# Kernel optimization log

Measured on AMD Instinct MI355X. Metric: run time of the kernel, lower is better.

The kernel has to match this reference:

```python
import jax, jax.numpy as jnp
import numpy as np
import math

EMBED_DIM = 512
NHEAD = 8
HEAD_DIM = EMBED_DIM // NHEAD
B, L = 32, 512
EPS = 1e-5


def layer_norm(x, gamma, beta):
    mu = jnp.mean(x, axis=-1, keepdims=True)
    var = jnp.var(x, axis=-1, keepdims=True)
    return (x - mu) * jax.lax.rsqrt(var + EPS) * gamma + beta


def setup_inputs() -> dict:
    key = jax.random.key(0)
    ks = jax.random.split(key, 16)
    D = EMBED_DIM
    s = 1.0 / math.sqrt(D)
    return {
        "x": jax.random.normal(ks[0], (B, L, D), dtype=jnp.float32),
        "inter": jax.random.normal(ks[1], (B, L, L, 4), dtype=jnp.float32),
        "qkv_w": jax.random.normal(ks[2], (D, 3 * D), dtype=jnp.float32) * s,
        "qkv_b": jnp.zeros((3 * D,), dtype=jnp.float32),
        "out_w": jax.random.normal(ks[3], (D, D), dtype=jnp.float32) * s,
        "out_b": jnp.zeros((D,), dtype=jnp.float32),
        "norm1_g": jnp.ones((D,), dtype=jnp.float32),
        "norm1_b": jnp.zeros((D,), dtype=jnp.float32),
        "norm2_g": jnp.ones((D,), dtype=jnp.float32),
        "norm2_b": jnp.zeros((D,), dtype=jnp.float32),
        "inter_w": jax.random.normal(ks[4], (4, NHEAD), dtype=jnp.float32) * 0.5,
        "ffn_w1": jax.random.normal(ks[5], (D, 4 * D), dtype=jnp.float32) * s,
        "ffn_b1": jnp.zeros((4 * D,), dtype=jnp.float32),
        "ffn_w2": jax.random.normal(ks[6], (4 * D, D), dtype=jnp.float32) * (1.0 / math.sqrt(4 * D)),
        "ffn_b2": jnp.zeros((D,), dtype=jnp.float32),
    }


def reference(x, inter, qkv_w, qkv_b, out_w, out_b, norm1_g, norm1_b,
              norm2_g, norm2_b, inter_w, ffn_w1, ffn_b1, ffn_w2, ffn_b2):
    Bb, Ll, D = x.shape
    residual = x
    h = layer_norm(x, norm1_g, norm1_b)
    qkv = (h @ qkv_w + qkv_b).reshape(Bb, Ll, 3, NHEAD, HEAD_DIM)
    qkv = jnp.transpose(qkv, (2, 0, 3, 1, 4))  # (3, B, H, L, hd)
    q, k, v = qkv[0], qkv[1], qkv[2]
    scale = math.sqrt(HEAD_DIM)
    scores = jnp.einsum("bhqd,bhkd->bhqk", q, k) / scale
    # pairwise interaction bias: (B,L,L,4) @ (4,H) -> (B,H,L,L)
    bias = jnp.einsum("bqkf,fh->bhqk", inter, inter_w)
    attn = jax.nn.softmax(scores + bias, axis=-1)
    # dropout p=0 in eval mode
    out = jnp.einsum("bhqk,bhkd->bhqd", attn, v)
    out = jnp.transpose(out, (0, 2, 1, 3)).reshape(Bb, Ll, D)
    x = residual + out @ out_w + out_b
    h2 = layer_norm(x, norm2_g, norm2_b)
    ffn = jax.nn.gelu(h2 @ ffn_w1 + ffn_b1, approximate=False) @ ffn_w2 + ffn_b2
    return x + ffn
```

## Files before the change

kernel.cpp:

```cpp
#include <hip/hip_runtime.h>
#include <math.h>

#define BB 32
#define LL 512
#define DD 512
#define NH 8
#define HD 64

typedef __attribute__((ext_vector_type(8))) short bf16x8;
typedef __attribute__((ext_vector_type(4))) float f32x4;

__device__ __forceinline__ unsigned short f2bf(float x) {
    union { float f; unsigned u; } v; v.f = x;
    unsigned r = v.u + 0x7fffu + ((v.u >> 16) & 1u);
    return (unsigned short)(r >> 16);
}

__device__ __forceinline__ float warp_sum(float v) {
    #pragma unroll
    for (int o = 32; o > 0; o >>= 1) v += __shfl_down(v, o);
    return v;
}

__global__ void ln_kernel(const float* __restrict__ X, const float* __restrict__ g,
                          const float* __restrict__ b, unsigned short* __restrict__ Y) {
    __shared__ float red[8];
    const size_t base = (size_t)blockIdx.x * DD;
    const int t = threadIdx.x;
    float x0 = X[base + t], x1 = X[base + t + 256];
    float s = warp_sum(x0 + x1);
    float q = warp_sum(x0 * x0 + x1 * x1);
    if ((t & 63) == 0) { red[t >> 6] = s; red[4 + (t >> 6)] = q; }
    __syncthreads();
    float S = red[0] + red[1] + red[2] + red[3];
    float Q = red[4] + red[5] + red[6] + red[7];
    float mu  = S * (1.0f / 512.0f);
    float var = Q * (1.0f / 512.0f) - mu * mu;
    float r = rsqrtf(var + 1e-5f);
    Y[base + t]       = f2bf((x0 - mu) * r * g[t] + b[t]);
    Y[base + t + 256] = f2bf((x1 - mu) * r * g[t + 256] + b[t + 256]);
}

__global__ void transpose_bf16(const float* __restrict__ W, unsigned short* __restrict__ WT,
                               int K, int N) {
    __shared__ float t[32][33];
    const int n0 = blockIdx.x * 32, k0 = blockIdx.y * 32;
    const int tx = threadIdx.x & 31, ty = threadIdx.x >> 5;
    #pragma unroll
    for (int r = 0; r < 32; r += 8)
        t[ty + r][tx] = W[(size_t)(k0 + ty + r) * N + n0 + tx];
    __syncthreads();
    #pragma unroll
    for (int r = 0; r < 32; r += 8)
        WT[(size_t)(n0 + ty + r) * K + k0 + tx] = f2bf(t[tx][ty + r]);
}

template <int ACT, int RES, int OM>
__global__ __launch_bounds__(256)
void gemm_mfma(const unsigned short* __restrict__ A, const unsigned short* __restrict__ BT,
               const float* __restrict__ bias, const float* __restrict__ res,
               void* __restrict__ Cv, unsigned short* __restrict__ kfrag,
               unsigned short* __restrict__ vfrag, int M, int N, int K) {
    __shared__ unsigned short As0[128 * 64];
    __shared__ unsigned short Bs0[128 * 64];
    __shared__ unsigned short As1[128 * 64];
    __shared__ unsigned short Bs1[128 * 64];
    const int tid = threadIdx.x;
    const int wave = tid >> 6, lane = tid & 63;
    const int wm = (wave >> 1) * 64, wn = (wave & 1) * 64;

    const int nx = N >> 7;
    const int chunk = (int)gridDim.x >> 3;
    const int o = ((int)blockIdx.x & 7) * chunk + ((int)blockIdx.x >> 3);
    const int bn = (o % nx) * 128;
    const int bm = (o / nx) * 128;

    f32x4 acc[4][4] = {};

    auto stage = [&](unsigned short* AS, unsigned short* BS, int k0) {
        #pragma unroll
        for (int it = 0; it < 4; ++it) {
            const int s = it * 256 + tid;
            const int row = s >> 3, pch = s & 7;
            const int lch = pch ^ (row & 7);
            const unsigned short* ga = A + (size_t)(bm + row) * K + k0 + lch * 8;
            __builtin_amdgcn_global_load_lds(
                (const __attribute__((address_space(1))) void*)ga,
                (__attribute__((address_space(3))) void*)(AS + s * 8), 16, 0, 0);
            const unsigned short* gb = BT + (size_t)(bn + row) * K + k0 + lch * 8;
            __builtin_amdgcn_global_load_lds(
                (const __attribute__((address_space(1))) void*)gb,
                (__attribute__((address_space(3))) void*)(BS + s * 8), 16, 0, 0);
        }
    };

    auto compute = [&](const unsigned short* AS, const unsigned short* BS) {
        #pragma unroll
        for (int ks = 0; ks < 2; ++ks) {
            bf16x8 af[4], bfr[4];
            #pragma unroll
            for (int i = 0; i < 4; ++i) {
                const int row = wm + i * 16 + (lane & 15);
                const int pch = (ks * 4 + (lane >> 4)) ^ (row & 7);
                af[i] = *(const bf16x8*)(AS + row * 64 + pch * 8);
            }
            #pragma unroll
            for (int j = 0; j < 4; ++j) {
                const int row = wn + j * 16 + (lane & 15);
                const int pch = (ks * 4 + (lane >> 4)) ^ (row & 7);
                bfr[j] = *(const bf16x8*)(BS + row * 64 + pch * 8);
            }
            #pragma unroll
            for (int i = 0; i < 4; ++i)
                #pragma unroll
                for (int j = 0; j < 4; ++j)
                    acc[i][j] = __builtin_amdgcn_mfma_f32_16x16x32_bf16(
                        af[i], bfr[j], acc[i][j], 0, 0, 0);
        }
    };

    stage(As0, Bs0, 0);
    for (int k0 = 0; k0 < K; k0 += 128) {
        __syncthreads();
        if (k0 + 64 < K) stage(As1, Bs1, k0 + 64);
        compute(As0, Bs0);
        __syncthreads();
        if (k0 + 128 < K) stage(As0, Bs0, k0 + 128);
        compute(As1, Bs1);
    }

    const int cl = lane & 15, rq = (lane >> 4) * 4;
    #pragma unroll
    for (int j = 0; j < 4; ++j) {
        const int col = bn + wn + j * 16 + cl;
        const float bv = bias[col];
        #pragma unroll
        for (int i = 0; i < 4; ++i) {
            const int r0 = bm + wm + i * 16 + rq;
            #pragma unroll
            for (int r = 0; r < 4; ++r) {
                float v = acc[i][j][r] + bv;
                if (ACT == 1) v = 0.5f * v * (1.0f + erff(v * 0.70710678118654752f));
                if (RES) v += res[(size_t)(r0 + r) * N + col];
                if (OM == 0) {
                    ((float*)Cv)[(size_t)(r0 + r) * N + col] = v;
                } else if (OM == 1) {
                    ((unsigned short*)Cv)[(size_t)(r0 + r) * N + col] = f2bf(v);
                } else {
                    const int row = r0 + r;
                    const int b = row >> 9, kpos = row & 511;
                    if (col < 512) {
                        ((unsigned short*)Cv)[(size_t)row * 512 + col] = f2bf(v * 0.125f);
                    } else if (col < 1024) {
                        const int h = (col - 512) >> 6, dd = (col - 512) & 63;
                        const int kt = kpos >> 6, jj = (kpos >> 4) & 3, lo2 = kpos & 15;
                        const int kk = dd >> 5, hi2 = (dd >> 3) & 3, e = dd & 7;
                        kfrag[((((size_t)(b * NH + h) * 8 + kt) * 2 + kk) * 4 + jj) * 512
                              + (hi2 * 16 + lo2) * 8 + e] = f2bf(v);
                    } else {
                        const int h = (col - 1024) >> 6, dd = (col - 1024) & 63;
                        const int kt = kpos >> 6, kk = (kpos >> 5) & 1, hi2 = (kpos >> 3) & 3, e = kpos & 7;
                        const int jj = dd >> 4, lo2 = dd & 15;
                        vfrag[((((size_t)(b * NH + h) * 8 + kt) * 2 + kk) * 4 + jj) * 512
                              + (hi2 * 16 + lo2) * 8 + e] = f2bf(v);
                    }
                }
            }
        }
    }
}

__global__ __launch_bounds__(512)
void flash_kernel(const unsigned short* __restrict__ qbuf,
                  const unsigned short* __restrict__ kfrag,
                  const unsigned short* __restrict__ vfrag,
                  const float* __restrict__ inter,
                  const float* __restrict__ iw,
                  unsigned short* __restrict__ O) {
    __shared__ float it[2][16 * 256];
    __shared__ unsigned short plds[8][16 * 72];
    const int qg = blockIdx.x, b = blockIdx.y;
    const int tid = threadIdx.x, wave = tid >> 6, lane = tid & 63;
    const int h = wave;
    const int lo = lane & 15, hi = lane >> 4;

    const float iw0 = iw[h], iw1 = iw[8 + h], iw2 = iw[16 + h], iw3 = iw[24 + h];
    const float* interb = inter + (size_t)b * 512 * 512 * 4;
    unsigned short* pw = &plds[wave][0];

    const unsigned short* qp = qbuf + ((size_t)(b * 512 + qg * 16 + lo)) * 512 + h * 64 + hi * 8;
    const bf16x8 qf0 = *(const bf16x8*)(qp);
    const bf16x8 qf1 = *(const bf16x8*)(qp + 32);

    const unsigned short* kfb = kfrag + (size_t)(b * NH + h) * 32768 + (size_t)lane * 8;
    const unsigned short* vfb = vfrag + (size_t)(b * NH + h) * 32768 + (size_t)lane * 8;

    const int srow0 = wave * 2, srow1 = wave * 2 + 1;
    const float* sg0 = interb + (((size_t)(qg * 16 + srow0)) * 512 + (lane ^ (srow0 & 7))) * 4;
    const float* sg1 = interb + (((size_t)(qg * 16 + srow1)) * 512 + (lane ^ (srow1 & 7))) * 4;

    f32x4 o[4] = {};
    float m = -1e30f, lsum = 0.0f;

    bf16x8 kf[8];
    #pragma unroll
    for (int jj = 0; jj < 8; ++jj)
        kf[jj] = *(const bf16x8*)(kfb + jj * 512);
    __builtin_amdgcn_global_load_lds(
        (const __attribute__((address_space(1))) void*)sg0,
        (__attribute__((address_space(3))) void*)(&it[0][srow0 * 256] + lane * 4), 16, 0, 0);
    __builtin_amdgcn_global_load_lds(
        (const __attribute__((address_space(1))) void*)sg1,
        (__attribute__((address_space(3))) void*)(&it[0][srow1 * 256] + lane * 4), 16, 0, 0);

    #pragma unroll 1
    for (int kt = 0; kt < 8; ++kt) {
        const int buf = kt & 1;
        __syncthreads();
        f32x4 s4[4] = {};
        __builtin_amdgcn_s_setprio(1);
        #pragma unroll
        for (int j = 0; j < 4; ++j)
            s4[j] = __builtin_amdgcn_mfma_f32_16x16x32_bf16(kf[j], qf0, s4[j], 0, 0, 0);
        #pragma unroll
        for (int j = 0; j < 4; ++j)
            s4[j] = __builtin_amdgcn_mfma_f32_16x16x32_bf16(kf[4 + j], qf1, s4[j], 0, 0, 0);
        __builtin_amdgcn_s_setprio(0);
        const unsigned short* vp = vfb + kt * 4096;
        bf16x8 vf[8];
        #pragma unroll
        for (int jj = 0; jj < 8; ++jj)
            vf[jj] = *(const bf16x8*)(vp + jj * 512);
        if (kt < 7) {
            const unsigned short* kp = kfb + (kt + 1) * 4096;
            #pragma unroll
            for (int jj = 0; jj < 8; ++jj)
                kf[jj] = *(const bf16x8*)(kp + jj * 512);
        }
        if (kt < 7) {
            const int kb2 = (kt + 1) * 64;
            __builtin_amdgcn_global_load_lds(
                (const __attribute__((address_space(1))) void*)(sg0 + kb2 * 4),
                (__attribute__((address_space(3))) void*)(&it[buf ^ 1][srow0 * 256] + lane * 4),
                16, 0, 0);
            __builtin_amdgcn_global_load_lds(
                (const __attribute__((address_space(1))) void*)(sg1 + kb2 * 4),
                (__attribute__((address_space(3))) void*)(&it[buf ^ 1][srow1 * 256] + lane * 4),
                16, 0, 0);
        }
        __builtin_amdgcn_sched_barrier(0);
        {
            const float* bb = &it[buf][lo * 256];
            const int x7 = lo & 7;
            #pragma unroll
            for (int j = 0; j < 4; ++j) {
                #pragma unroll
                for (int r = 0; r < 4; ++r) {
                    const int c = (((hi * 4 + r) ^ x7) + j * 16) * 4;
                    const float4 f = *(const float4*)(bb + c);
                    s4[j][r] = s4[j][r] + f.x * iw0 + f.y * iw1 + f.z * iw2 + f.w * iw3;
                }
            }
        }
        float t0 = fmaxf(fmaxf(s4[0][0], s4[0][1]), fmaxf(s4[0][2], s4[0][3]));
        float t1 = fmaxf(fmaxf(s4[1][0], s4[1][1]), fmaxf(s4[1][2], s4[1][3]));
        float t2 = fmaxf(fmaxf(s4[2][0], s4[2][1]), fmaxf(s4[2][2], s4[2][3]));
        float t3 = fmaxf(fmaxf(s4[3][0], s4[3][1]), fmaxf(s4[3][2], s4[3][3]));
        float mx = fmaxf(fmaxf(t0, t1), fmaxf(t2, t3));
        mx = fmaxf(mx, __shfl_xor(mx, 16));
        mx = fmaxf(mx, __shfl_xor(mx, 32));
        const float mn = fmaxf(m, mx);
        const float al = __expf(m - mn);
        m = mn;
        #pragma unroll
        for (int j = 0; j < 4; ++j)
            #pragma unroll
            for (int r = 0; r < 4; ++r)
                s4[j][r] = __expf(s4[j][r] - mn);
        float u0 = (s4[0][0] + s4[0][1]) + (s4[0][2] + s4[0][3]);
        float u1 = (s4[1][0] + s4[1][1]) + (s4[1][2] + s4[1][3]);
        float u2 = (s4[2][0] + s4[2][1]) + (s4[2][2] + s4[2][3]);
        float u3 = (s4[3][0] + s4[3][1]) + (s4[3][2] + s4[3][3]);
        float ts = (u0 + u1) + (u2 + u3);
        ts += __shfl_xor(ts, 16);
        ts += __shfl_xor(ts, 32);
        lsum = lsum * al + ts;
        const float aR0 = __shfl(al, hi * 4 + 0);
        const float aR1 = __shfl(al, hi * 4 + 1);
        const float aR2 = __shfl(al, hi * 4 + 2);
        const float aR3 = __shfl(al, hi * 4 + 3);
        #pragma unroll
        for (int j2 = 0; j2 < 4; ++j2) {
            o[j2][0] *= aR0; o[j2][1] *= aR1; o[j2][2] *= aR2; o[j2][3] *= aR3;
        }
        uint2* pq = (uint2*)(pw + lo * 72);
        #pragma unroll
        for (int j = 0; j < 4; ++j) {
            uint2 d;
            d.x = (unsigned)f2bf(s4[j][0]) | ((unsigned)f2bf(s4[j][1]) << 16);
            d.y = (unsigned)f2bf(s4[j][2]) | ((unsigned)f2bf(s4[j][3]) << 16);
            pq[j * 4 + hi] = d;
        }
        __builtin_amdgcn_s_setprio(1);
        #pragma unroll
        for (int kk = 0; kk < 2; ++kk) {
            const bf16x8 pf = *(const bf16x8*)(pw + lo * 72 + kk * 32 + hi * 8);
            #pragma unroll
            for (int j2 = 0; j2 < 4; ++j2)
                o[j2] = __builtin_amdgcn_mfma_f32_16x16x32_bf16(
                    pf, vf[kk * 4 + j2], o[j2], 0, 0, 0);
        }
        __builtin_amdgcn_s_setprio(0);
    }

    const float iR0 = 1.0f / __shfl(lsum, hi * 4 + 0);
    const float iR1 = 1.0f / __shfl(lsum, hi * 4 + 1);
    const float iR2 = 1.0f / __shfl(lsum, hi * 4 + 2);
    const float iR3 = 1.0f / __shfl(lsum, hi * 4 + 3);
    const int qC0 = qg * 16 + hi * 4;
    #pragma unroll
    for (int j2 = 0; j2 < 4; ++j2) {
        O[(size_t)(b * 512 + qC0 + 0) * 512 + h * 64 + j2 * 16 + lo] = f2bf(o[j2][0] * iR0);
        O[(size_t)(b * 512 + qC0 + 1) * 512 + h * 64 + j2 * 16 + lo] = f2bf(o[j2][1] * iR1);
        O[(size_t)(b * 512 + qC0 + 2) * 512 + h * 64 + j2 * 16 + lo] = f2bf(o[j2][2] * iR2);
        O[(size_t)(b * 512 + qC0 + 3) * 512 + h * 64 + j2 * 16 + lo] = f2bf(o[j2][3] * iR3);
    }
}

extern "C" void kernel_launch(void* const* d_in, const int* in_sizes, int n_in,
                              void* d_out, int out_size, void* d_ws, size_t ws_size,
                              hipStream_t stream) {
    const float* x     = (const float*)d_in[0];
    const float* inter = (const float*)d_in[1];
    const float* qkv_w = (const float*)d_in[2];
    const float* qkv_b = (const float*)d_in[3];
    const float* out_w = (const float*)d_in[4];
    const float* out_b = (const float*)d_in[5];
    const float* n1g   = (const float*)d_in[6];
    const float* n1b   = (const float*)d_in[7];
    const float* n2g   = (const float*)d_in[8];
    const float* n2b   = (const float*)d_in[9];
    const float* iw    = (const float*)d_in[10];
    const float* fw1   = (const float*)d_in[11];
    const float* fb1   = (const float*)d_in[12];
    const float* fw2   = (const float*)d_in[13];
    const float* fb2   = (const float*)d_in[14];
    float* out = (float*)d_out;

    if (ws_size < 190840832ull) return;
    char* ws = (char*)d_ws;
    unsigned short* qbuf    = (unsigned short*)(ws);
    unsigned short* kfrag   = (unsigned short*)(ws + 16777216ull);
    unsigned short* vfrag   = (unsigned short*)(ws + 33554432ull);
    unsigned short* attnout = (unsigned short*)(ws + 50331648ull);
    float*          x2      = (float*)(ws + 67108864ull);
    unsigned short* h_bf    = (unsigned short*)(ws + 100663296ull);
    unsigned short* ffnmid  = (unsigned short*)(ws + 117440512ull);
    unsigned short* qkv_wT  = (unsigned short*)(ws + 184549376ull);
    unsigned short* out_wT  = (unsigned short*)(ws + 186122240ull);
    unsigned short* fw1T    = (unsigned short*)(ws + 186646528ull);
    unsigned short* fw2T    = (unsigned short*)(ws + 188743680ull);

    const int M = BB * LL;

    transpose_bf16<<<dim3(1536 / 32, 512 / 32), 256, 0, stream>>>(qkv_w, qkv_wT, 512, 1536);
    transpose_bf16<<<dim3(512 / 32, 512 / 32), 256, 0, stream>>>(out_w, out_wT, 512, 512);
    transpose_bf16<<<dim3(2048 / 32, 512 / 32), 256, 0, stream>>>(fw1, fw1T, 512, 2048);
    transpose_bf16<<<dim3(512 / 32, 2048 / 32), 256, 0, stream>>>(fw2, fw2T, 2048, 512);
    ln_kernel<<<M, 256, 0, stream>>>(x, n1g, n1b, h_bf);
    gemm_mfma<0, 0, 2><<<dim3((1536 / 128) * (M / 128)), 256, 0, stream>>>(
        h_bf, qkv_wT, qkv_b, nullptr, qbuf, kfrag, vfrag, M, 1536, 512);
    flash_kernel<<<dim3(LL / 16, BB), 512, 0, stream>>>(qbuf, kfrag, vfrag, inter, iw, attnout);
    gemm_mfma<0, 1, 0><<<dim3((512 / 128) * (M / 128)), 256, 0, stream>>>(
        attnout, out_wT, out_b, x, x2, nullptr, nullptr, M, 512, 512);
    ln_kernel<<<M, 256, 0, stream>>>(x2, n2g, n2b, h_bf);
    gemm_mfma<1, 0, 1><<<dim3((2048 / 128) * (M / 128)), 256, 0, stream>>>(
        h_bf, fw1T, fb1, nullptr, ffnmid, nullptr, nullptr, M, 2048, 512);
    gemm_mfma<0, 1, 0><<<dim3((512 / 128) * (M / 128)), 256, 0, stream>>>(
        ffnmid, fw2T, fb2, x2, out, nullptr, nullptr, M, 512, 2048);
}
```

Measured before the change: 543.7 us.

## Use 256x256 GEMM tiles for QKV and FFN1, restructure flash K/V loads

Adds a 512-thread GEMM variant with 256x256 output tiles, used for the QKV projection and first FFN GEMM. Each wave computes 128x64, which raises the MFMA-to-LDS-load ratio and halves global re-reads of the operands. The cost is 128 KB of LDS per block and more accumulator registers, so occupancy drops and there are fewer blocks to spread over the CUs. The flash kernel now loads K and V fragments at the top of each iteration instead of prefetching the next K tile, which lowers register pressure but exposes more load latency.

```diff
diff --git a/kernel.cpp b/kernel.cpp
--- a/kernel.cpp
+++ b/kernel.cpp
@@ -56,6 +56,37 @@
 }
 
 template <int ACT, int RES, int OM>
+__device__ __forceinline__ void epi_store(
+    float v, int row, int col, int N,
+    const float* __restrict__ res, void* __restrict__ Cv,
+    unsigned short* __restrict__ kfrag, unsigned short* __restrict__ vfrag) {
+    if (ACT == 1) v = 0.5f * v * (1.0f + erff(v * 0.70710678118654752f));
+    if (RES) v += res[(size_t)row * N + col];
+    if (OM == 0) {
+        ((float*)Cv)[(size_t)row * N + col] = v;
+    } else if (OM == 1) {
+        ((unsigned short*)Cv)[(size_t)row * N + col] = f2bf(v);
+    } else {
+        const int b = row >> 9, kpos = row & 511;
+        if (col < 512) {
+            ((unsigned short*)Cv)[(size_t)row * 512 + col] = f2bf(v * 0.125f);
+        } else if (col < 1024) {
+            const int h = (col - 512) >> 6, dd = (col - 512) & 63;
+            const int kt = kpos >> 6, jj = (kpos >> 4) & 3, lo2 = kpos & 15;
+            const int kk = dd >> 5, hi2 = (dd >> 3) & 3, e = dd & 7;
+            kfrag[((((size_t)(b * NH + h) * 8 + kt) * 2 + kk) * 4 + jj) * 512
+                  + (hi2 * 16 + lo2) * 8 + e] = f2bf(v);
+        } else {
+            const int h = (col - 1024) >> 6, dd = (col - 1024) & 63;
+            const int kt = kpos >> 6, kk = (kpos >> 5) & 1, hi2 = (kpos >> 3) & 3, e = kpos & 7;
+            const int jj = dd >> 4, lo2 = dd & 15;
+            vfrag[((((size_t)(b * NH + h) * 8 + kt) * 2 + kk) * 4 + jj) * 512
+                  + (hi2 * 16 + lo2) * 8 + e] = f2bf(v);
+        }
+    }
+}
+
+template <int ACT, int RES, int OM>
 __global__ __launch_bounds__(256)
 void gemm_mfma(const unsigned short* __restrict__ A, const unsigned short* __restrict__ BT,
                const float* __restrict__ bias, const float* __restrict__ res,
@@ -138,34 +169,98 @@
         for (int i = 0; i < 4; ++i) {
             const int r0 = bm + wm + i * 16 + rq;
             #pragma unroll
-            for (int r = 0; r < 4; ++r) {
-                float v = acc[i][j][r] + bv;
-                if (ACT == 1) v = 0.5f * v * (1.0f + erff(v * 0.70710678118654752f));
-                if (RES) v += res[(size_t)(r0 + r) * N + col];
-                if (OM == 0) {
-                    ((float*)Cv)[(size_t)(r0 + r) * N + col] = v;
-                } else if (OM == 1) {
-                    ((unsigned short*)Cv)[(size_t)(r0 + r) * N + col] = f2bf(v);
-                } else {
-                    const int row = r0 + r;
-                    const int b = row >> 9, kpos = row & 511;
-                    if (col < 512) {
-                        ((unsigned short*)Cv)[(size_t)row * 512 + col] = f2bf(v * 0.125f);
-                    } else if (col < 1024) {
-                        const int h = (col - 512) >> 6, dd = (col - 512) & 63;
-                        const int kt = kpos >> 6, jj = (kpos >> 4) & 3, lo2 = kpos & 15;
-                        const int kk = dd >> 5, hi2 = (dd >> 3) & 3, e = dd & 7;
-                        kfrag[((((size_t)(b * NH + h) * 8 + kt) * 2 + kk) * 4 + jj) * 512
-                              + (hi2 * 16 + lo2) * 8 + e] = f2bf(v);
-                    } else {
-                        const int h = (col - 1024) >> 6, dd = (col - 1024) & 63;
-                        const int kt = kpos >> 6, kk = (kpos >> 5) & 1, hi2 = (kpos >> 3) & 3, e = kpos & 7;
-                        const int jj = dd >> 4, lo2 = dd & 15;
-                        vfrag[((((size_t)(b * NH + h) * 8 + kt) * 2 + kk) * 4 + jj) * 512
-                              + (hi2 * 16 + lo2) * 8 + e] = f2bf(v);
-                    }
-                }
+            for (int r = 0; r < 4; ++r)
+                epi_store<ACT, RES, OM>(acc[i][j][r] + bv, r0 + r, col, N, res, Cv, kfrag, vfrag);
+        }
+    }
+}
+
+template <int ACT, int OM>
+__global__ __launch_bounds__(512, 2)
+void gemm_mfma256(const unsigned short* __restrict__ A, const unsigned short* __restrict__ BT,
+                  const float* __restrict__ bias, void* __restrict__ Cv,
+                  unsigned short* __restrict__ kfrag, unsigned short* __restrict__ vfrag,
+                  int M, int N, int K) {
+    __shared__ unsigned short As0[256 * 64];
+    __shared__ unsigned short Bs0[256 * 64];
+    __shared__ unsigned short As1[256 * 64];
+    __shared__ unsigned short Bs1[256 * 64];
+    const int tid = threadIdx.x;
+    const int wave = tid >> 6, lane = tid & 63;
+    const int wm = (wave >> 2) * 128, wn = (wave & 3) * 64;
+
+    const int nx = N >> 8;
+    const int chunk = (int)gridDim.x >> 3;
+    const int o = ((int)blockIdx.x & 7) * chunk + ((int)blockIdx.x >> 3);
+    const int bn = (o % nx) * 256;
+    const int bm = (o / nx) * 256;
+
+    f32x4 acc[8][4] = {};
+
+    auto stage = [&](unsigned short* AS, unsigned short* BS, int k0) {
+        #pragma unroll
+        for (int it = 0; it < 4; ++it) {
+            const int s = it * 512 + tid;
+            const int row = s >> 3, pch = s & 7;
+            const int lch = pch ^ (row & 7);
+            const unsigned short* ga = A + (size_t)(bm + row) * K + k0 + lch * 8;
+            __builtin_amdgcn_global_load_lds(
+                (const __attribute__((address_space(1))) void*)ga,
+                (__attribute__((address_space(3))) void*)(AS + s * 8), 16, 0, 0);
+            const unsigned short* gb = BT + (size_t)(bn + row) * K + k0 + lch * 8;
+            __builtin_amdgcn_global_load_lds(
+                (const __attribute__((address_space(1))) void*)gb,
+                (__attribute__((address_space(3))) void*)(BS + s * 8), 16, 0, 0);
+        }
+    };
+
+    auto compute = [&](const unsigned short* AS, const unsigned short* BS) {
+        #pragma unroll
+        for (int ks = 0; ks < 2; ++ks) {
+            bf16x8 bfr[4];
+            #pragma unroll
+            for (int j = 0; j < 4; ++j) {
+                const int row = wn + j * 16 + (lane & 15);
+                const int pch = (ks * 4 + (lane >> 4)) ^ (row & 7);
+                bfr[j] = *(const bf16x8*)(BS + row * 64 + pch * 8);
             }
+            bf16x8 af[8];
+            #pragma unroll
+            for (int i = 0; i < 8; ++i) {
+                const int row = wm + i * 16 + (lane & 15);
+                const int pch = (ks * 4 + (lane >> 4)) ^ (row & 7);
+                af[i] = *(const bf16x8*)(AS + row * 64 + pch * 8);
+            }
+            #pragma unroll
+            for (int i = 0; i < 8; ++i)
+                #pragma unroll
+                for (int j = 0; j < 4; ++j)
+                    acc[i][j] = __builtin_amdgcn_mfma_f32_16x16x32_bf16(
+                        af[i], bfr[j], acc[i][j], 0, 0, 0);
+        }
+    };
+
+    stage(As0, Bs0, 0);
+    for (int k0 = 0; k0 < K; k0 += 128) {
+        __syncthreads();
+        if (k0 + 64 < K) stage(As1, Bs1, k0 + 64);
+        compute(As0, Bs0);
+        __syncthreads();
+        if (k0 + 128 < K) stage(As0, Bs0, k0 + 128);
+        compute(As1, Bs1);
+    }
+
+    const int cl = lane & 15, rq = (lane >> 4) * 4;
+    #pragma unroll
+    for (int j = 0; j < 4; ++j) {
+        const int col = bn + wn + j * 16 + cl;
+        const float bv = bias[col];
+        #pragma unroll
+        for (int i = 0; i < 8; ++i) {
+            const int r0 = bm + wm + i * 16 + rq;
+            #pragma unroll
+            for (int r = 0; r < 4; ++r)
+                epi_store<ACT, 0, OM>(acc[i][j][r] + bv, r0 + r, col, N, nullptr, Cv, kfrag, vfrag);
         }
     }
 }
@@ -202,10 +297,6 @@
     f32x4 o[4] = {};
     float m = -1e30f, lsum = 0.0f;
 
-    bf16x8 kf[8];
-    #pragma unroll
-    for (int jj = 0; jj < 8; ++jj)
-        kf[jj] = *(const bf16x8*)(kfb + jj * 512);
     __builtin_amdgcn_global_load_lds(
         (const __attribute__((address_space(1))) void*)sg0,
         (__attribute__((address_space(3))) void*)(&it[0][srow0 * 256] + lane * 4), 16, 0, 0);
@@ -217,6 +308,28 @@
     for (int kt = 0; kt < 8; ++kt) {
         const int buf = kt & 1;
         __syncthreads();
+        const unsigned short* kp = kfb + kt * 4096;
+        bf16x8 kf[8];
+        #pragma unroll
+        for (int jj = 0; jj < 8; ++jj)
+            kf[jj] = *(const bf16x8*)(kp + jj * 512);
+        const unsigned short* vp = vfb + kt * 4096;
+        bf16x8 vf[8];
+        #pragma unroll
+        for (int jj = 0; jj < 8; ++jj)
+            vf[jj] = *(const bf16x8*)(vp + jj * 512);
+        if (kt < 7) {
+            const int kb2 = (kt + 1) * 64;
+            __builtin_amdgcn_global_load_lds(
+                (const __attribute__((address_space(1))) void*)(sg0 + kb2 * 4),
+                (__attribute__((address_space(3))) void*)(&it[buf ^ 1][srow0 * 256] + lane * 4),
+                16, 0, 0);
+            __builtin_amdgcn_global_load_lds(
+                (const __attribute__((address_space(1))) void*)(sg1 + kb2 * 4),
+                (__attribute__((address_space(3))) void*)(&it[buf ^ 1][srow1 * 256] + lane * 4),
+                16, 0, 0);
+        }
+        __builtin_amdgcn_sched_barrier(0);
         f32x4 s4[4] = {};
         __builtin_amdgcn_s_setprio(1);
         #pragma unroll
@@ -226,29 +339,6 @@
         for (int j = 0; j < 4; ++j)
             s4[j] = __builtin_amdgcn_mfma_f32_16x16x32_bf16(kf[4 + j], qf1, s4[j], 0, 0, 0);
         __builtin_amdgcn_s_setprio(0);
-        const unsigned short* vp = vfb + kt * 4096;
-        bf16x8 vf[8];
-        #pragma unroll
-        for (int jj = 0; jj < 8; ++jj)
-            vf[jj] = *(const bf16x8*)(vp + jj * 512);
-        if (kt < 7) {
-            const unsigned short* kp = kfb + (kt + 1) * 4096;
-            #pragma unroll
-            for (int jj = 0; jj < 8; ++jj)
-                kf[jj] = *(const bf16x8*)(kp + jj * 512);
-        }
-        if (kt < 7) {
-            const int kb2 = (kt + 1) * 64;
-            __builtin_amdgcn_global_load_lds(
-                (const __attribute__((address_space(1))) void*)(sg0 + kb2 * 4),
-                (__attribute__((address_space(3))) void*)(&it[buf ^ 1][srow0 * 256] + lane * 4),
-                16, 0, 0);
-            __builtin_amdgcn_global_load_lds(
-                (const __attribute__((address_space(1))) void*)(sg1 + kb2 * 4),
-                (__attribute__((address_space(3))) void*)(&it[buf ^ 1][srow1 * 256] + lane * 4),
-                16, 0, 0);
-        }
-        __builtin_amdgcn_sched_barrier(0);
         {
             const float* bb = &it[buf][lo * 256];
             const int x7 = lo & 7;
@@ -368,14 +458,14 @@
     transpose_bf16<<<dim3(2048 / 32, 512 / 32), 256, 0, stream>>>(fw1, fw1T, 512, 2048);
     transpose_bf16<<<dim3(512 / 32, 2048 / 32), 256, 0, stream>>>(fw2, fw2T, 2048, 512);
     ln_kernel<<<M, 256, 0, stream>>>(x, n1g, n1b, h_bf);
-    gemm_mfma<0, 0, 2><<<dim3((1536 / 128) * (M / 128)), 256, 0, stream>>>(
-        h_bf, qkv_wT, qkv_b, nullptr, qbuf, kfrag, vfrag, M, 1536, 512);
+    gemm_mfma256<0, 2><<<dim3((1536 / 256) * (M / 256)), 512, 0, stream>>>(
+        h_bf, qkv_wT, qkv_b, qbuf, kfrag, vfrag, M, 1536, 512);
     flash_kernel<<<dim3(LL / 16, BB), 512, 0, stream>>>(qbuf, kfrag, vfrag, inter, iw, attnout);
     gemm_mfma<0, 1, 0><<<dim3((512 / 128) * (M / 128)), 256, 0, stream>>>(
         attnout, out_wT, out_b, x, x2, nullptr, nullptr, M, 512, 512);
     ln_kernel<<<M, 256, 0, stream>>>(x2, n2g, n2b, h_bf);
-    gemm_mfma<1, 0, 1><<<dim3((2048 / 128) * (M / 128)), 256, 0, stream>>>(
-        h_bf, fw1T, fb1, nullptr, ffnmid, nullptr, nullptr, M, 2048, 512);
+    gemm_mfma256<1, 1><<<dim3((2048 / 256) * (M / 256)), 512, 0, stream>>>(
+        h_bf, fw1T, fb1, ffnmid, nullptr, nullptr, M, 2048, 512);
     gemm_mfma<0, 1, 0><<<dim3((512 / 128) * (M / 128)), 256, 0, stream>>>(
         ffnmid, fw2T, fb2, x2, out, nullptr, nullptr, M, 512, 2048);
 }
```

Measured after the change: 535.0 us. About the same (-1.6%).
